# Kernel optimization log

Hardware: AMD Instinct MI355X
Metric: run time of the kernel (lower is better)

Reference implementation:

```python
import jax, jax.numpy as jnp
import numpy as np
from jax import lax

VOCAB, EMB, HID, T, B, NCLS = 30000, 100, 128, 200, 512, 9
BN_EPS = 1e-3  # keras BatchNormalization default epsilon


def _lstm(x, W, U, b, reverse):
    # Keras LSTM with activation='relu', recurrent_activation='sigmoid'.
    # x: [B,T,E]; W: [E,4H]; U: [H,4H]; b: [4H]. Gate order: i, f, c, o.
    xz = jnp.einsum('bte,eh->bth', x, W) + b  # precompute input projection [B,T,4H]
    H = U.shape[0]
    Bsz = x.shape[0]

    def step(carry, xz_t):
        h, c = carry
        z = xz_t + h @ U
        zi, zf, zg, zo = jnp.split(z, 4, axis=-1)
        i = jax.nn.sigmoid(zi)
        f = jax.nn.sigmoid(zf)
        g = jax.nn.relu(zg)          # activation='relu' on candidate
        o = jax.nn.sigmoid(zo)
        c = f * c + i * g
        h = o * jax.nn.relu(c)       # activation='relu' on cell output
        return (h, c), h

    init = (jnp.zeros((Bsz, H), x.dtype), jnp.zeros((Bsz, H), x.dtype))
    _, hs = lax.scan(step, init, jnp.swapaxes(xz, 0, 1), reverse=reverse)
    return jnp.swapaxes(hs, 0, 1)  # [B,T,H]


def setup_inputs() -> dict:
    key = jax.random.key(0)
    ks = jax.random.split(key, 12)
    s = 0.05
    return {
        'tokens': jax.random.randint(ks[0], (B, T), 0, VOCAB, dtype=jnp.int32),
        'emb': jax.random.normal(ks[1], (VOCAB, EMB), jnp.float32) * s,
        'Wf': jax.random.normal(ks[2], (EMB, 4 * HID), jnp.float32) * s,
        'Uf': jax.random.normal(ks[3], (HID, 4 * HID), jnp.float32) * s,
        'bf': jnp.zeros((4 * HID,), jnp.float32),
        'Wb': jax.random.normal(ks[4], (EMB, 4 * HID), jnp.float32) * s,
        'Ub': jax.random.normal(ks[5], (HID, 4 * HID), jnp.float32) * s,
        'bb': jnp.zeros((4 * HID,), jnp.float32),
        'gamma': jnp.ones((2 * HID,), jnp.float32),
        'beta': jnp.zeros((2 * HID,), jnp.float32),
        'mov_mean': jax.random.normal(ks[6], (2 * HID,), jnp.float32) * 0.01,
        'mov_var': jnp.ones((2 * HID,), jnp.float32),
        'Wd': jax.random.normal(ks[7], (2 * HID, NCLS), jnp.float32) * s,
        'bd': jnp.zeros((NCLS,), jnp.float32),
    }


def reference(tokens, emb, Wf, Uf, bf, Wb, Ub, bb, gamma, beta, mov_mean, mov_var, Wd, bd):
    x = emb[tokens]                                   # [B,T,EMB]
    h_fwd = _lstm(x, Wf, Uf, bf, reverse=False)       # [B,T,HID]
    h_bwd = _lstm(x, Wb, Ub, bb, reverse=True)        # [B,T,HID]
    h = jnp.concatenate([h_fwd, h_bwd], axis=-1)      # [B,T,2H]
    # BatchNormalization (inference mode, moving stats), dropout is identity at inference
    h = (h - mov_mean) * lax.rsqrt(mov_var + BN_EPS) * gamma + beta
    return jax.nn.softmax(h @ Wd + bd, axis=-1)       # [B,T,NCLS]
```

## Files before the change

### kernel.cpp

```cpp
#include <hip/hip_runtime.h>


#define TT 200

typedef short v8s __attribute__((ext_vector_type(8)));
typedef float v4f __attribute__((ext_vector_type(4)));

__device__ __forceinline__ void block_sync_lds() {
    asm volatile("s_waitcnt lgkmcnt(0)\n\ts_barrier" ::: "memory");
}
__device__ __forceinline__ float bf2f(unsigned short u) {
    unsigned x = ((unsigned)u) << 16;
    return __builtin_bit_cast(float, x);
}
__device__ __forceinline__ unsigned short f2bf(float f) {
    unsigned u = __builtin_bit_cast(unsigned, f);
    u += 0x7fffu + ((u >> 16) & 1u);
    return (unsigned short)(u >> 16);
}
__device__ __forceinline__ float clampf(float x, float c) {
    return fminf(fmaxf(x, -c), c);
}
__device__ __forceinline__ float sigmf(float x) {
    return __builtin_amdgcn_rcpf(1.0f + __expf(-x));
}
__device__ __forceinline__ bool probe_f32(const void* mvar) {
    return *(const unsigned*)mvar == 0x3F800000u;
}
__device__ __forceinline__ float ldf(const void* p, int i, bool f32) {
    return f32 ? ((const float*)p)[i] : bf2f(((const unsigned short*)p)[i]);
}

__global__ __launch_bounds__(256) void k_cast(const void* __restrict__ emb,
                                              const void* __restrict__ mvar,
                                              unsigned short* __restrict__ emb_b) {
    bool f32 = probe_f32(mvar);
    int n = 3000000;
    for (int i = blockIdx.x * 256 + threadIdx.x; i < n; i += gridDim.x * 256)
        emb_b[i] = f32 ? f2bf(((const float*)emb)[i]) : ((const unsigned short*)emb)[i];
}

__global__ __launch_bounds__(512) void k_prep(
    const void* __restrict__ Wf, const void* __restrict__ Uf,
    const void* __restrict__ Wb, const void* __restrict__ Ub,
    const void* __restrict__ gamma, const void* __restrict__ beta,
    const void* __restrict__ mmean, const void* __restrict__ mvar,
    const void* __restrict__ Wd, const void* __restrict__ bd,
    const void* __restrict__ bfv, const void* __restrict__ bbv,
    unsigned short* __restrict__ WU_T, unsigned short* __restrict__ WlT,
    float* __restrict__ bias_c, float* __restrict__ bdp) {
    bool f32 = probe_f32(mvar);
    int bid = blockIdx.x, tid = threadIdx.x;
    if (bid < 128) {
        int e0 = bid * 2048 + tid * 4;
        int dir = e0 >> 17;
        int n = (e0 >> 8) & 511;
        int k0 = e0 & 255;
        const void* W = dir ? Wb : Wf;
        const void* U = dir ? Ub : Uf;
        unsigned short v[4];
#pragma unroll
        for (int i = 0; i < 4; i++) {
            int k = k0 + i;
            float x = (k < 100) ? ldf(W, k * 512 + n, f32)
                    : (k < 128) ? 0.0f
                                : ldf(U, (k - 128) * 512 + n, f32);
            v[i] = f2bf(x);
        }
        uint2 pk;
        pk.x = (unsigned)v[0] | ((unsigned)v[1] << 16);
        pk.y = (unsigned)v[2] | ((unsigned)v[3] << 16);
        *(uint2*)(WU_T + e0) = pk;
    } else if (bid == 128) {
#pragma unroll
        for (int e = 0; e < 8; e++) {
            int f = tid * 8 + e;
            int dir = f >> 11, j = (f >> 7) & 15, k = f & 127;
            int c = dir * 128 + k;
            unsigned short v = 0;
            if (j < 9) {
                float sc = ldf(gamma, c, f32) * rsqrtf(ldf(mvar, c, f32) + 1e-3f);
                v = f2bf(clampf(sc * ldf(Wd, c * 9 + j, f32), 1e4f));
            }
            WlT[f] = v;
        }
    } else {
        bias_c[tid] = ldf(bfv, tid, f32);
        bias_c[512 + tid] = ldf(bbv, tid, f32);
        if (tid < 9) {
            int j = tid;
            float acc = ldf(bd, j, f32);
            for (int c = 0; c < 256; c++) {
                float sc = ldf(gamma, c, f32) * rsqrtf(ldf(mvar, c, f32) + 1e-3f);
                float sh = ldf(beta, c, f32) - ldf(mmean, c, f32) * sc;
                acc += sh * ldf(Wd, c * 9 + j, f32);
            }
            bdp[j] = clampf(acc, 1e4f);
        }
    }
}

__global__ __launch_bounds__(256, 1) void k_lstm(
    const int* __restrict__ tokens, const unsigned short* __restrict__ emb,
    const unsigned short* __restrict__ WU_T, const unsigned short* __restrict__ WlT,
    const float* __restrict__ bias_c, float* __restrict__ part) {
    __shared__ __attribute__((aligned(16))) unsigned short h_lds[16][16][136];
    __shared__ __attribute__((aligned(16))) unsigned short wl_lds[2048];
    __shared__ int tok_lds[16 * TT];

    int tid = threadIdx.x;
    int w = tid >> 6, l = tid & 63;
    int quad = l >> 4, mrow = l & 15;
    int dir = blockIdx.x >> 5, rb = blockIdx.x & 31;
    int tbase = mrow * TT;

    v8s Bfr[8][8];
#pragma unroll
    for (int q = 0; q < 8; q++) {
        int n = (q >> 1) * 128 + w * 32 + (q & 1) * 16 + mrow;
        const unsigned short* base = WU_T + ((size_t)(dir * 512 + n)) * 256 + quad * 8;
#pragma unroll
        for (int s = 0; s < 8; s++) Bfr[q][s] = *(const v8s*)(base + s * 32);
    }
    v4f bacc[8];
#pragma unroll
    for (int q = 0; q < 8; q++) {
        float b = bias_c[dir * 512 + (q >> 1) * 128 + w * 32 + (q & 1) * 16 + mrow];
        bacc[q] = (v4f){b, b, b, b};
    }

    for (int i = tid; i < 16 * 16 * 136; i += 256) ((unsigned short*)h_lds)[i] = 0;
    for (int i = tid; i < 2048; i += 256) wl_lds[i] = WlT[dir * 2048 + i];
    {
        const int* tsrc = tokens + (size_t)rb * 16 * TT;
        for (int i = tid; i < 16 * TT; i += 256) tok_lds[i] = tsrc[i];
    }
    __syncthreads();

    float cst[8] = {0.f, 0.f, 0.f, 0.f, 0.f, 0.f, 0.f, 0.f};
    float* ppart = part + (size_t)dir * (102400u * 12u);

#define GATHER_X(d0, d1, d2, d3, step)                                             \
    {                                                                              \
        int tpos = dir ? (TT - 1 - (step)) : (step);                               \
        int tok = tok_lds[tbase + tpos];                                           \
        const unsigned short* er = emb + (size_t)tok * 100 + quad * 8;             \
        union { uint2 u[2]; v8s v; } a0, a1, a2, a3;                               \
        a0.u[0] = *(const uint2*)er;        a0.u[1] = *(const uint2*)(er + 4);     \
        a1.u[0] = *(const uint2*)(er + 32); a1.u[1] = *(const uint2*)(er + 36);    \
        a2.u[0] = *(const uint2*)(er + 64); a2.u[1] = *(const uint2*)(er + 68);    \
        a3.u[0] = make_uint2(0u, 0u); a3.u[1] = make_uint2(0u, 0u);                \
        if (quad == 0) a3.u[0] = *(const uint2*)(emb + (size_t)tok * 100 + 96);    \
        d0 = a0.v; d1 = a1.v; d2 = a2.v; d3 = a3.v;                                \
    }

#define XPART(AN, X0, X1, X2, X3)                                                  \
    {                                                                              \
        _Pragma("unroll") for (int q = 0; q < 8; q++)                              \
            AN[q] = __builtin_amdgcn_mfma_f32_16x16x32_bf16(X0, Bfr[q][0], bacc[q], 0, 0, 0); \
        _Pragma("unroll") for (int q = 0; q < 8; q++)                              \
            AN[q] = __builtin_amdgcn_mfma_f32_16x16x32_bf16(X1, Bfr[q][1], AN[q], 0, 0, 0);   \
        _Pragma("unroll") for (int q = 0; q < 8; q++)                              \
            AN[q] = __builtin_amdgcn_mfma_f32_16x16x32_bf16(X2, Bfr[q][2], AN[q], 0, 0, 0);   \
        _Pragma("unroll") for (int q = 0; q < 8; q++)                              \
            AN[q] = __builtin_amdgcn_mfma_f32_16x16x32_bf16(X3, Bfr[q][3], AN[q], 0, 0, 0);   \
    }

#define HPART(AC, h0, h1, h2, h3)                                                  \
    {                                                                              \
        _Pragma("unroll") for (int q = 0; q < 8; q++)                              \
            AC[q] = __builtin_amdgcn_mfma_f32_16x16x32_bf16(h0, Bfr[q][4], AC[q], 0, 0, 0); \
        _Pragma("unroll") for (int q = 0; q < 8; q++)                              \
            AC[q] = __builtin_amdgcn_mfma_f32_16x16x32_bf16(h1, Bfr[q][5], AC[q], 0, 0, 0); \
        _Pragma("unroll") for (int q = 0; q < 8; q++)                              \
            AC[q] = __builtin_amdgcn_mfma_f32_16x16x32_bf16(h2, Bfr[q][6], AC[q], 0, 0, 0); \
        _Pragma("unroll") for (int q = 0; q < 8; q++)                              \
            AC[q] = __builtin_amdgcn_mfma_f32_16x16x32_bf16(h3, Bfr[q][7], AC[q], 0, 0, 0); \
    }

#define LOGITS(ITV)                                                                \
    {                                                                              \
        const unsigned short* wbase = wl_lds + mrow * 128 + quad * 8;              \
        v8s wl0 = *(const v8s*)(wbase);                                            \
        v8s wl1 = *(const v8s*)(wbase + 32);                                       \
        v8s wl2 = *(const v8s*)(wbase + 64);                                       \
        v8s wl3 = *(const v8s*)(wbase + 96);                                       \
        _Pragma("unroll") for (int g = 0; g < 2; g++) {                            \
            int s = (ITV)-8 + w + 4 * g;                                           \
            int sl = s & 15;                                                       \
            v8s hg0 = *(const v8s*)&h_lds[sl][mrow][quad * 8];                     \
            v8s hg1 = *(const v8s*)&h_lds[sl][mrow][32 + quad * 8];                \
            v8s hg2 = *(const v8s*)&h_lds[sl][mrow][64 + quad * 8];                \
            v8s hg3 = *(const v8s*)&h_lds[sl][mrow][96 + quad * 8];                \
            v4f la = {0.f, 0.f, 0.f, 0.f};                                         \
            la = __builtin_amdgcn_mfma_f32_16x16x32_bf16(hg0, wl0, la, 0, 0, 0);   \
            la = __builtin_amdgcn_mfma_f32_16x16x32_bf16(hg1, wl1, la, 0, 0, 0);   \
            la = __builtin_amdgcn_mfma_f32_16x16x32_bf16(hg2, wl2, la, 0, 0, 0);   \
            la = __builtin_amdgcn_mfma_f32_16x16x32_bf16(hg3, wl3, la, 0, 0, 0);   \
            if (mrow < 9) {                                                        \
                int tpos = dir ? (TT - 1 - s) : s;                                 \
                float* pp = ppart + ((size_t)(rb * 16 + quad * 4) * TT + tpos) * 12 + mrow; \
                _Pragma("unroll") for (int r = 0; r < 4; r++) pp[r * (TT * 12)] = la[r];    \
            }                                                                      \
        }                                                                          \
    }

#define STEP(ITV, AC, AN, XC0, XC1, XC2, XC3, XN0, XN1, XN2, XN3, DOLOG)           \
    {                                                                              \
        if ((ITV) + 2 < TT) GATHER_X(XN0, XN1, XN2, XN3, (ITV) + 2);               \
        if (DOLOG && (ITV) && (((ITV) & 7) == 0)) LOGITS(ITV);                     \
        int rs = ((ITV)-1) & 15;                                                   \
        v8s ha0 = *(const v8s*)&h_lds[rs][mrow][quad * 8];                         \
        v8s ha1 = *(const v8s*)&h_lds[rs][mrow][32 + quad * 8];                    \
        v8s ha2 = *(const v8s*)&h_lds[rs][mrow][64 + quad * 8];                    \
        v8s ha3 = *(const v8s*)&h_lds[rs][mrow][96 + quad * 8];                    \
        if ((ITV) + 1 < TT) XPART(AN, XC0, XC1, XC2, XC3);                         \
        HPART(AC, ha0, ha1, ha2, ha3);                                             \
        int ws = (ITV) & 15;                                                       \
        _Pragma("unroll") for (int nt = 0; nt < 2; nt++) {                         \
            _Pragma("unroll") for (int r = 0; r < 4; r++) {                        \
                float i_ = sigmf(AC[nt][r]);                                       \
                float f_ = sigmf(AC[2 + nt][r]);                                   \
                float g_ = fmaxf(AC[4 + nt][r], 0.0f);                             \
                float o_ = sigmf(AC[6 + nt][r]);                                   \
                float c_ = f_ * cst[nt * 4 + r] + i_ * g_;                         \
                cst[nt * 4 + r] = c_;                                              \
                h_lds[ws][quad * 4 + r][w * 32 + nt * 16 + mrow] =                 \
                    f2bf(o_ * fmaxf(c_, 0.0f));                                    \
            }                                                                      \
        }                                                                          \
        block_sync_lds();                                                          \
    }

    v8s xA0, xA1, xA2, xA3, xB0, xB1, xB2, xB3;
    v4f accA[8], accB[8];
    GATHER_X(xA0, xA1, xA2, xA3, 0);
    XPART(accA, xA0, xA1, xA2, xA3);
    GATHER_X(xB0, xB1, xB2, xB3, 1);

    for (int it = 0; it < TT; it += 2) {
        STEP(it, accA, accB, xB0, xB1, xB2, xB3, xA0, xA1, xA2, xA3, 1);
        STEP(it + 1, accB, accA, xA0, xA1, xA2, xA3, xB0, xB1, xB2, xB3, 0);
    }
    LOGITS(TT);
#undef GATHER_X
#undef XPART
#undef HPART
#undef LOGITS
#undef STEP
}

__global__ __launch_bounds__(256) void k_head(const float* __restrict__ part,
                                              const float* __restrict__ bdp,
                                              float* __restrict__ out) {
    int tid = threadIdx.x;
    int tok0 = blockIdx.x * 256 + tid;
    float bias[9];
#pragma unroll
    for (int j = 0; j < 9; j++) bias[j] = bdp[j];
#pragma unroll
    for (int u = 0; u < 2; u++) {
        int tok = tok0 + u * 51200;
        const float* p0 = part + (size_t)tok * 12;
        const float* p1 = part + (size_t)(102400 + tok) * 12;
        v4f a0 = *(const v4f*)p0, a1 = *(const v4f*)(p0 + 4);
        float a8 = p0[8];
        v4f b0 = *(const v4f*)p1, b1 = *(const v4f*)(p1 + 4);
        float b8 = p1[8];
        float lg[9];
#pragma unroll
        for (int j = 0; j < 4; j++) lg[j] = clampf(a0[j] + b0[j] + bias[j], 1e4f);
#pragma unroll
        for (int j = 0; j < 4; j++) lg[4 + j] = clampf(a1[j] + b1[j] + bias[4 + j], 1e4f);
        lg[8] = clampf(a8 + b8 + bias[8], 1e4f);
        float m = lg[0];
#pragma unroll
        for (int j = 1; j < 9; j++) m = fmaxf(m, lg[j]);
        float e[9], s = 0.f;
#pragma unroll
        for (int j = 0; j < 9; j++) { e[j] = __expf(lg[j] - m); s += e[j]; }
        float r = 1.0f / s;
        size_t base = (size_t)tok * 9;
#pragma unroll
        for (int j = 0; j < 9; j++) out[base + j] = e[j] * r;
    }
}

extern "C" void kernel_launch(void* const* d_in, const int* in_sizes, int n_in,
                              void* d_out, int out_size, void* d_ws, size_t ws_size,
                              hipStream_t stream) {
    const int* tokens = (const int*)d_in[0];
    const void* emb = d_in[1];
    const void* Wf = d_in[2];
    const void* Uf = d_in[3];
    const void* bfv = d_in[4];
    const void* Wb = d_in[5];
    const void* Ub = d_in[6];
    const void* bbv = d_in[7];
    const void* gamma = d_in[8];
    const void* beta = d_in[9];
    const void* mmean = d_in[10];
    const void* mvar = d_in[11];
    const void* Wd = d_in[12];
    const void* bd = d_in[13];

    char* ws = (char*)d_ws;
    unsigned short* WU_T = (unsigned short*)ws;
    unsigned short* WlT = (unsigned short*)(ws + 524288);
    float* bias_c = (float*)(ws + 532480);
    float* bdp = (float*)(ws + 536576);
    unsigned short* emb_b = (unsigned short*)(ws + 536640);
    float* part = (float*)(ws + 6536640);

    k_cast<<<1024, 256, 0, stream>>>(emb, mvar, emb_b);
    k_prep<<<130, 512, 0, stream>>>(Wf, Uf, Wb, Ub, gamma, beta, mmean, mvar, Wd, bd,
                                    bfv, bbv, WU_T, WlT, bias_c, bdp);
    k_lstm<<<64, 256, 0, stream>>>(tokens, emb_b, WU_T, WlT, bias_c, part);
    k_head<<<200, 256, 0, stream>>>(part, bdp, (float*)d_out);
}
```

Before: 451.7 us.

## Split LSTM block into producer warps for input projection and gate warps

Blocks grow from 256 to 1024 threads. Eight warps compute the input projection x·W plus bias and the logits, writing projections into a double-buffered LDS area. The other eight warps run the recurrent h·U matmul and the gate update, each owning 16 hidden columns instead of 32, which halves the serial per-step work on the critical path. The cost is LDS traffic for the projected inputs and fewer registers per thread, with one barrier per step across 16 warps. Token storage in LDS is narrowed to 16-bit.

```diff
diff --git a/kernel.cpp b/kernel.cpp
--- a/kernel.cpp
+++ b/kernel.cpp
@@ -100,50 +100,65 @@
     }
 }
 
-__global__ __launch_bounds__(256, 1) void k_lstm(
+__global__ __launch_bounds__(1024, 1) void k_lstm(
     const int* __restrict__ tokens, const unsigned short* __restrict__ emb,
     const unsigned short* __restrict__ WU_T, const unsigned short* __restrict__ WlT,
     const float* __restrict__ bias_c, float* __restrict__ part) {
     __shared__ __attribute__((aligned(16))) unsigned short h_lds[16][16][136];
-    __shared__ __attribute__((aligned(16))) unsigned short wl_lds[2048];
-    __shared__ int tok_lds[16 * TT];
+    __shared__ __attribute__((aligned(16))) float accx_lds[2][512][16];
+    __shared__ unsigned short tok_lds[16 * TT];
 
     int tid = threadIdx.x;
-    int w = tid >> 6, l = tid & 63;
+    int w16 = tid >> 6, l = tid & 63;
     int quad = l >> 4, mrow = l & 15;
+    int w = w16 & 7;
+    bool xw = w16 >= 8;
     int dir = blockIdx.x >> 5, rb = blockIdx.x & 31;
     int tbase = mrow * TT;
-
-    v8s Bfr[8][8];
-#pragma unroll
-    for (int q = 0; q < 8; q++) {
-        int n = (q >> 1) * 128 + w * 32 + (q & 1) * 16 + mrow;
-        const unsigned short* base = WU_T + ((size_t)(dir * 512 + n)) * 256 + quad * 8;
-#pragma unroll
-        for (int s = 0; s < 8; s++) Bfr[q][s] = *(const v8s*)(base + s * 32);
-    }
-    v4f bacc[8];
-#pragma unroll
-    for (int q = 0; q < 8; q++) {
-        float b = bias_c[dir * 512 + (q >> 1) * 128 + w * 32 + (q & 1) * 16 + mrow];
-        bacc[q] = (v4f){b, b, b, b};
-    }
-
-    for (int i = tid; i < 16 * 16 * 136; i += 256) ((unsigned short*)h_lds)[i] = 0;
-    for (int i = tid; i < 2048; i += 256) wl_lds[i] = WlT[dir * 2048 + i];
+    int nbase = w * 16 + mrow;
+
+    v8s Bh[4][4];
+    v8s Bx[4][4];
+    v4f bacc[4];
+    v8s Wl[4];
+    float cst[4] = {0.f, 0.f, 0.f, 0.f};
+
+    if (!xw) {
+#pragma unroll
+        for (int G = 0; G < 4; G++) {
+            int n = G * 128 + nbase;
+            const unsigned short* base = WU_T + ((size_t)(dir * 512 + n)) * 256 + quad * 8;
+#pragma unroll
+            for (int s = 0; s < 4; s++) Bh[G][s] = *(const v8s*)(base + (4 + s) * 32);
+        }
+    } else {
+#pragma unroll
+        for (int G = 0; G < 4; G++) {
+            int n = G * 128 + nbase;
+            const unsigned short* base = WU_T + ((size_t)(dir * 512 + n)) * 256 + quad * 8;
+#pragma unroll
+            for (int s = 0; s < 4; s++) Bx[G][s] = *(const v8s*)(base + s * 32);
+            float b = bias_c[dir * 512 + n];
+            bacc[G] = (v4f){b, b, b, b};
+        }
+        const unsigned short* wbase = WlT + dir * 2048 + mrow * 128 + quad * 8;
+#pragma unroll
+        for (int s = 0; s < 4; s++) Wl[s] = *(const v8s*)(wbase + s * 32);
+    }
+
+    for (int i = tid; i < 16 * 16 * 136; i += 1024) ((unsigned short*)h_lds)[i] = 0;
     {
         const int* tsrc = tokens + (size_t)rb * 16 * TT;
-        for (int i = tid; i < 16 * TT; i += 256) tok_lds[i] = tsrc[i];
+        for (int i = tid; i < 16 * TT; i += 1024) tok_lds[i] = (unsigned short)tsrc[i];
     }
     __syncthreads();
 
-    float cst[8] = {0.f, 0.f, 0.f, 0.f, 0.f, 0.f, 0.f, 0.f};
     float* ppart = part + (size_t)dir * (102400u * 12u);
 
 #define GATHER_X(d0, d1, d2, d3, step)                                             \
     {                                                                              \
         int tpos = dir ? (TT - 1 - (step)) : (step);                               \
-        int tok = tok_lds[tbase + tpos];                                           \
+        int tok = (int)tok_lds[tbase + tpos];                                      \
         const unsigned short* er = emb + (size_t)tok * 100 + quad * 8;             \
         union { uint2 u[2]; v8s v; } a0, a1, a2, a3;                               \
         a0.u[0] = *(const uint2*)er;        a0.u[1] = *(const uint2*)(er + 4);     \
@@ -154,100 +169,101 @@
         d0 = a0.v; d1 = a1.v; d2 = a2.v; d3 = a3.v;                                \
     }
 
-#define XPART(AN, X0, X1, X2, X3)                                                  \
-    {                                                                              \
-        _Pragma("unroll") for (int q = 0; q < 8; q++)                              \
-            AN[q] = __builtin_amdgcn_mfma_f32_16x16x32_bf16(X0, Bfr[q][0], bacc[q], 0, 0, 0); \
-        _Pragma("unroll") for (int q = 0; q < 8; q++)                              \
-            AN[q] = __builtin_amdgcn_mfma_f32_16x16x32_bf16(X1, Bfr[q][1], AN[q], 0, 0, 0);   \
-        _Pragma("unroll") for (int q = 0; q < 8; q++)                              \
-            AN[q] = __builtin_amdgcn_mfma_f32_16x16x32_bf16(X2, Bfr[q][2], AN[q], 0, 0, 0);   \
-        _Pragma("unroll") for (int q = 0; q < 8; q++)                              \
-            AN[q] = __builtin_amdgcn_mfma_f32_16x16x32_bf16(X3, Bfr[q][3], AN[q], 0, 0, 0);   \
-    }
-
-#define HPART(AC, h0, h1, h2, h3)                                                  \
-    {                                                                              \
-        _Pragma("unroll") for (int q = 0; q < 8; q++)                              \
-            AC[q] = __builtin_amdgcn_mfma_f32_16x16x32_bf16(h0, Bfr[q][4], AC[q], 0, 0, 0); \
-        _Pragma("unroll") for (int q = 0; q < 8; q++)                              \
-            AC[q] = __builtin_amdgcn_mfma_f32_16x16x32_bf16(h1, Bfr[q][5], AC[q], 0, 0, 0); \
-        _Pragma("unroll") for (int q = 0; q < 8; q++)                              \
-            AC[q] = __builtin_amdgcn_mfma_f32_16x16x32_bf16(h2, Bfr[q][6], AC[q], 0, 0, 0); \
-        _Pragma("unroll") for (int q = 0; q < 8; q++)                              \
-            AC[q] = __builtin_amdgcn_mfma_f32_16x16x32_bf16(h3, Bfr[q][7], AC[q], 0, 0, 0); \
+#define XPART_STORE(X0, X1, X2, X3, SLOT)                                          \
+    {                                                                              \
+        v4f AN[4];                                                                 \
+        _Pragma("unroll") for (int G = 0; G < 4; G++)                              \
+            AN[G] = __builtin_amdgcn_mfma_f32_16x16x32_bf16(X0, Bx[G][0], bacc[G], 0, 0, 0); \
+        _Pragma("unroll") for (int G = 0; G < 4; G++)                              \
+            AN[G] = __builtin_amdgcn_mfma_f32_16x16x32_bf16(X1, Bx[G][1], AN[G], 0, 0, 0);   \
+        _Pragma("unroll") for (int G = 0; G < 4; G++)                              \
+            AN[G] = __builtin_amdgcn_mfma_f32_16x16x32_bf16(X2, Bx[G][2], AN[G], 0, 0, 0);   \
+        _Pragma("unroll") for (int G = 0; G < 4; G++)                              \
+            AN[G] = __builtin_amdgcn_mfma_f32_16x16x32_bf16(X3, Bx[G][3], AN[G], 0, 0, 0);   \
+        _Pragma("unroll") for (int G = 0; G < 4; G++)                              \
+            *(v4f*)&accx_lds[SLOT][G * 128 + nbase][quad * 4] = AN[G];             \
     }
 
 #define LOGITS(ITV)                                                                \
     {                                                                              \
-        const unsigned short* wbase = wl_lds + mrow * 128 + quad * 8;              \
-        v8s wl0 = *(const v8s*)(wbase);                                            \
-        v8s wl1 = *(const v8s*)(wbase + 32);                                       \
-        v8s wl2 = *(const v8s*)(wbase + 64);                                       \
-        v8s wl3 = *(const v8s*)(wbase + 96);                                       \
-        _Pragma("unroll") for (int g = 0; g < 2; g++) {                            \
-            int s = (ITV)-8 + w + 4 * g;                                           \
-            int sl = s & 15;                                                       \
-            v8s hg0 = *(const v8s*)&h_lds[sl][mrow][quad * 8];                     \
-            v8s hg1 = *(const v8s*)&h_lds[sl][mrow][32 + quad * 8];                \
-            v8s hg2 = *(const v8s*)&h_lds[sl][mrow][64 + quad * 8];                \
-            v8s hg3 = *(const v8s*)&h_lds[sl][mrow][96 + quad * 8];                \
-            v4f la = {0.f, 0.f, 0.f, 0.f};                                         \
-            la = __builtin_amdgcn_mfma_f32_16x16x32_bf16(hg0, wl0, la, 0, 0, 0);   \
-            la = __builtin_amdgcn_mfma_f32_16x16x32_bf16(hg1, wl1, la, 0, 0, 0);   \
-            la = __builtin_amdgcn_mfma_f32_16x16x32_bf16(hg2, wl2, la, 0, 0, 0);   \
-            la = __builtin_amdgcn_mfma_f32_16x16x32_bf16(hg3, wl3, la, 0, 0, 0);   \
-            if (mrow < 9) {                                                        \
-                int tpos = dir ? (TT - 1 - s) : s;                                 \
-                float* pp = ppart + ((size_t)(rb * 16 + quad * 4) * TT + tpos) * 12 + mrow; \
-                _Pragma("unroll") for (int r = 0; r < 4; r++) pp[r * (TT * 12)] = la[r];    \
-            }                                                                      \
+        int s = (ITV)-8 + w;                                                       \
+        int sl = s & 15;                                                           \
+        v8s hg0 = *(const v8s*)&h_lds[sl][mrow][quad * 8];                         \
+        v8s hg1 = *(const v8s*)&h_lds[sl][mrow][32 + quad * 8];                    \
+        v8s hg2 = *(const v8s*)&h_lds[sl][mrow][64 + quad * 8];                    \
+        v8s hg3 = *(const v8s*)&h_lds[sl][mrow][96 + quad * 8];                    \
+        v4f la = {0.f, 0.f, 0.f, 0.f};                                             \
+        la = __builtin_amdgcn_mfma_f32_16x16x32_bf16(hg0, Wl[0], la, 0, 0, 0);     \
+        la = __builtin_amdgcn_mfma_f32_16x16x32_bf16(hg1, Wl[1], la, 0, 0, 0);     \
+        la = __builtin_amdgcn_mfma_f32_16x16x32_bf16(hg2, Wl[2], la, 0, 0, 0);     \
+        la = __builtin_amdgcn_mfma_f32_16x16x32_bf16(hg3, Wl[3], la, 0, 0, 0);     \
+        if (mrow < 9) {                                                            \
+            int tpos = dir ? (TT - 1 - s) : s;                                     \
+            float* pp = ppart + ((size_t)(rb * 16 + quad * 4) * TT + tpos) * 12 + mrow; \
+            _Pragma("unroll") for (int r = 0; r < 4; r++) pp[r * (TT * 12)] = la[r];    \
         }                                                                          \
     }
 
-#define STEP(ITV, AC, AN, XC0, XC1, XC2, XC3, XN0, XN1, XN2, XN3, DOLOG)           \
+#define XSTEP(ITV, XC0, XC1, XC2, XC3, XN0, XN1, XN2, XN3)                         \
     {                                                                              \
         if ((ITV) + 2 < TT) GATHER_X(XN0, XN1, XN2, XN3, (ITV) + 2);               \
-        if (DOLOG && (ITV) && (((ITV) & 7) == 0)) LOGITS(ITV);                     \
+        if ((ITV) && (((ITV) & 7) == 0)) LOGITS(ITV);                              \
+        if ((ITV) + 1 < TT) XPART_STORE(XC0, XC1, XC2, XC3, ((ITV) + 1) & 1);      \
+    }
+
+#define GSTEP(ITV)                                                                 \
+    {                                                                              \
         int rs = ((ITV)-1) & 15;                                                   \
         v8s ha0 = *(const v8s*)&h_lds[rs][mrow][quad * 8];                         \
         v8s ha1 = *(const v8s*)&h_lds[rs][mrow][32 + quad * 8];                    \
         v8s ha2 = *(const v8s*)&h_lds[rs][mrow][64 + quad * 8];                    \
         v8s ha3 = *(const v8s*)&h_lds[rs][mrow][96 + quad * 8];                    \
-        if ((ITV) + 1 < TT) XPART(AN, XC0, XC1, XC2, XC3);                         \
-        HPART(AC, ha0, ha1, ha2, ha3);                                             \
-        int ws = (ITV) & 15;                                                       \
-        _Pragma("unroll") for (int nt = 0; nt < 2; nt++) {                         \
-            _Pragma("unroll") for (int r = 0; r < 4; r++) {                        \
-                float i_ = sigmf(AC[nt][r]);                                       \
-                float f_ = sigmf(AC[2 + nt][r]);                                   \
-                float g_ = fmaxf(AC[4 + nt][r], 0.0f);                             \
-                float o_ = sigmf(AC[6 + nt][r]);                                   \
-                float c_ = f_ * cst[nt * 4 + r] + i_ * g_;                         \
-                cst[nt * 4 + r] = c_;                                              \
-                h_lds[ws][quad * 4 + r][w * 32 + nt * 16 + mrow] =                 \
-                    f2bf(o_ * fmaxf(c_, 0.0f));                                    \
-            }                                                                      \
+        const float* ab = &accx_lds[(ITV)&1][nbase][quad * 4];                     \
+        v4f acc[4];                                                                \
+        _Pragma("unroll") for (int G = 0; G < 4; G++)                              \
+            acc[G] = *(const v4f*)(ab + G * (128 * 16));                           \
+        _Pragma("unroll") for (int G = 0; G < 4; G++)                              \
+            acc[G] = __builtin_amdgcn_mfma_f32_16x16x32_bf16(ha0, Bh[G][0], acc[G], 0, 0, 0); \
+        _Pragma("unroll") for (int G = 0; G < 4; G++)                              \
+            acc[G] = __builtin_amdgcn_mfma_f32_16x16x32_bf16(ha1, Bh[G][1], acc[G], 0, 0, 0); \
+        _Pragma("unroll") for (int G = 0; G < 4; G++)                              \
+            acc[G] = __builtin_amdgcn_mfma_f32_16x16x32_bf16(ha2, Bh[G][2], acc[G], 0, 0, 0); \
+        _Pragma("unroll") for (int G = 0; G < 4; G++)                              \
+            acc[G] = __builtin_amdgcn_mfma_f32_16x16x32_bf16(ha3, Bh[G][3], acc[G], 0, 0, 0); \
+        int wsl = (ITV) & 15;                                                      \
+        _Pragma("unroll") for (int r = 0; r < 4; r++) {                            \
+            float i_ = sigmf(acc[0][r]);                                           \
+            float f_ = sigmf(acc[1][r]);                                           \
+            float g_ = fmaxf(acc[2][r], 0.0f);                                     \
+            float o_ = sigmf(acc[3][r]);                                           \
+            float c_ = f_ * cst[r] + i_ * g_;                                      \
+            cst[r] = c_;                                                           \
+            h_lds[wsl][quad * 4 + r][nbase] = f2bf(o_ * fmaxf(c_, 0.0f));          \
         }                                                                          \
-        block_sync_lds();                                                          \
     }
 
     v8s xA0, xA1, xA2, xA3, xB0, xB1, xB2, xB3;
-    v4f accA[8], accB[8];
-    GATHER_X(xA0, xA1, xA2, xA3, 0);
-    XPART(accA, xA0, xA1, xA2, xA3);
-    GATHER_X(xB0, xB1, xB2, xB3, 1);
+    if (xw) {
+        GATHER_X(xA0, xA1, xA2, xA3, 0);
+        XPART_STORE(xA0, xA1, xA2, xA3, 0);
+        GATHER_X(xB0, xB1, xB2, xB3, 1);
+    }
+    block_sync_lds();
 
     for (int it = 0; it < TT; it += 2) {
-        STEP(it, accA, accB, xB0, xB1, xB2, xB3, xA0, xA1, xA2, xA3, 1);
-        STEP(it + 1, accB, accA, xA0, xA1, xA2, xA3, xB0, xB1, xB2, xB3, 0);
-    }
-    LOGITS(TT);
+        if (xw) { XSTEP(it, xB0, xB1, xB2, xB3, xA0, xA1, xA2, xA3); }
+        else    { GSTEP(it); }
+        block_sync_lds();
+        if (xw) { XSTEP(it + 1, xA0, xA1, xA2, xA3, xB0, xB1, xB2, xB3); }
+        else    { GSTEP(it + 1); }
+        block_sync_lds();
+    }
+    if (xw) LOGITS(TT);
 #undef GATHER_X
-#undef XPART
-#undef HPART
+#undef XPART_STORE
 #undef LOGITS
-#undef STEP
+#undef XSTEP
+#undef GSTEP
 }
 
 __global__ __launch_bounds__(256) void k_head(const float* __restrict__ part,
@@ -315,6 +331,6 @@
     k_cast<<<1024, 256, 0, stream>>>(emb, mvar, emb_b);
     k_prep<<<130, 512, 0, stream>>>(Wf, Uf, Wb, Ub, gamma, beta, mmean, mvar, Wd, bd,
                                     bfv, bbv, WU_T, WlT, bias_c, bdp);
-    k_lstm<<<64, 256, 0, stream>>>(tokens, emb_b, WU_T, WlT, bias_c, part);
+    k_lstm<<<64, 1024, 0, stream>>>(tokens, emb_b, WU_T, WlT, bias_c, part);
     k_head<<<200, 256, 0, stream>>>(part, bdp, (float*)d_out);
 }
```

New measurement: 1.421 ms. 3.15x slower.
